# Kernel optimization log

Hardware: AMD Instinct MI355X
Metric: run time of the kernel (lower is better)

## Reference

```python
import jax, jax.numpy as jnp
import numpy as np

NUM_EMBEDDINGS = 8192
EMBEDDING_DIM = 256


def setup_inputs() -> dict:
    key = jax.random.key(0)
    k1, k2 = jax.random.split(key)
    z = jax.random.normal(k1, (16, EMBEDDING_DIM, 32, 32), dtype=jnp.float32)
    # nn.Embedding default init: N(0, 1)
    emb_table = jax.random.normal(k2, (NUM_EMBEDDINGS, EMBEDDING_DIM), dtype=jnp.float32)
    return {"z": z, "emb_table": emb_table}


def reference(z, emb_table):
    # z: [B, D, H, W]; emb_table: [K, D]
    B, D, H, W = z.shape
    # flatten to per-token vectors: [B*H*W, D]
    zf = z.reshape(B, D, H * W).transpose(0, 2, 1).reshape(B * H * W, D)
    Wt = jax.lax.stop_gradient(emb_table)  # original detaches W for distance
    # argmin of mean squared distance == argmin of squared distance;
    # expand ||z - w||^2 = ||z||^2 - 2 z.w + ||w||^2 (avoid (N,K,D) expansion)
    z_sq = jnp.sum(zf * zf, axis=-1, keepdims=True)          # [N, 1]
    w_sq = jnp.sum(Wt * Wt, axis=-1)                          # [K]
    dists = z_sq - 2.0 * (zf @ Wt.T) + w_sq                   # [N, K]
    token_ids = jnp.argmin(dists, axis=-1)                    # [N]
    quantized = emb_table[token_ids]                          # [N, D] (differentiable gather)
    return quantized.reshape(B, H * W, D).transpose(0, 2, 1).reshape(B, D, H, W)
```

## Files before the change

### kernel.cpp

```cpp
#include <hip/hip_runtime.h>
#include <stdint.h>

#define DIM 256
#define NEMB 8192
#define NTOK 16384
#define HW 1024

typedef __attribute__((ext_vector_type(4))) int int4v;

__device__ __forceinline__ void async_cp16(void* lds, const void* g) {
  __builtin_amdgcn_global_load_lds(
      (const __attribute__((address_space(1))) unsigned int*)g,
      (__attribute__((address_space(3))) unsigned int*)lds, 16, 0, 0);
}
__device__ __forceinline__ int q0_of(float x) {
  int q = __float2int_rn(x * 20.0f);
  return q > 127 ? 127 : (q < -127 ? -127 : q);
}
__device__ __forceinline__ int q1_of(float x, int q0) {
  float e = x * 20.0f - (float)q0;
  int q = __float2int_rn(e * 128.0f);
  return q > 127 ? 127 : (q < -127 ? -127 : q);
}
__device__ __forceinline__ unsigned int pack4(int a, int b, int c, int d) {
  return (unsigned int)(a & 0xff) | ((unsigned int)(b & 0xff) << 8) |
         ((unsigned int)(c & 0xff) << 16) | ((unsigned int)(d & 0xff) << 24);
}

__global__ __launch_bounds__(256) void prep_kernel(
    const float* __restrict__ emb, unsigned int* __restrict__ q0w,
    unsigned int* __restrict__ q1w, int* __restrict__ iwsq2,
    const float* __restrict__ z, unsigned int* __restrict__ q0z,
    unsigned int* __restrict__ q1z) {
  __shared__ float tile[64][65];
  int tid = threadIdx.x;
  int lane = tid & 63;
  if (blockIdx.x < 2048) {
    int row = blockIdx.x * 4 + (tid >> 6);
    const float4 v = *(const float4*)(emb + (size_t)row * DIM + lane * 4);
    float s = v.x * v.x + v.y * v.y + v.z * v.z + v.w * v.w;
    int a0 = q0_of(v.x), b0 = q0_of(v.y), c0 = q0_of(v.z), d0 = q0_of(v.w);
    q0w[row * (DIM / 4) + lane] = pack4(a0, b0, c0, d0);
    q1w[row * (DIM / 4) + lane] =
        pack4(q1_of(v.x, a0), q1_of(v.y, b0), q1_of(v.z, c0), q1_of(v.w, d0));
#pragma unroll
    for (int off = 32; off > 0; off >>= 1) s += __shfl_xor(s, off, 64);
    if (lane == 0) iwsq2[row] = (int)rintf(s * 25600.0f) + 8192;
    return;
  }
  int idx = blockIdx.x - 2048;
  int b = idx >> 6, d0 = ((idx >> 4) & 3) * 64, hw0 = (idx & 15) * 64;
  int grp = tid >> 6;
  const float* src = z + (size_t)b * DIM * HW + hw0 + lane;
#pragma unroll
  for (int i = 0; i < 16; i++) {
    int dl = grp + i * 4;
    tile[dl][lane] = src[(size_t)(d0 + dl) * HW];
  }
  __syncthreads();
  int dq = tid & 15;
#pragma unroll
  for (int p = 0; p < 4; p++) {
    int n = (tid >> 4) + p * 16;
    float x0 = tile[dq * 4 + 0][n], x1 = tile[dq * 4 + 1][n];
    float x2 = tile[dq * 4 + 2][n], x3 = tile[dq * 4 + 3][n];
    int a0 = q0_of(x0), b0 = q0_of(x1), c0 = q0_of(x2), e0 = q0_of(x3);
    int token = b * HW + hw0 + n;
    size_t off = (size_t)token * (DIM / 4) + (d0 >> 2) + dq;
    q0z[off] = pack4(a0, b0, c0, e0);
    q1z[off] = pack4(q1_of(x0, a0), q1_of(x1, b0), q1_of(x2, c0), q1_of(x3, e0));
  }
}

__global__ __launch_bounds__(128, 2) void gemm_topk_kernel(
    const signed char* __restrict__ q0z, const signed char* __restrict__ q1z,
    const signed char* __restrict__ q0w, const signed char* __restrict__ q1w,
    const int* __restrict__ iwsq2, uint2* __restrict__ partials) {
  __shared__ __align__(16) signed char sB[2][4][16 * 128];

  const int bid = blockIdx.x;
  const int kq = bid & 7;
  const int tg = bid >> 3;
  const int tid = threadIdx.x;
  const int lane = tid & 63, w = tid >> 6;
  const int c = lane & 15, quad = lane >> 4;
  const int n0 = tg * 128;
  const int k0g = kq * 1024;

  int4v af0[4][4], af1[4][4];
#pragma unroll
  for (int t = 0; t < 4; t++) {
    const size_t arow = (size_t)(n0 + w * 64 + t * 16 + c) * DIM;
#pragma unroll
    for (int s = 0; s < 4; s++) {
      af0[t][s] = *(const int4v*)(q0z + arow + s * 64 + quad * 16);
      af1[t][s] = *(const int4v*)(q1z + arow + s * 64 + quad * 16);
    }
  }

  const int srow = tid >> 3;
  const int scl = ((tid & 7) ^ (srow & 7)) * 16;
  const signed char* p0 = q0w + (size_t)(k0g + srow) * DIM + scl;
  const signed char* p1 = q1w + (size_t)(k0g + srow) * DIM + scl;
  async_cp16(&sB[0][0][tid * 16], p0);
  async_cp16(&sB[0][1][tid * 16], p0 + 128);
  async_cp16(&sB[0][2][tid * 16], p1);
  async_cp16(&sB[0][3][tid * 16], p1 + 128);
  p0 += 16 * DIM;
  p1 += 16 * DIM;
  __syncthreads();

  unsigned int m1[16], m2[16];
#pragma unroll
  for (int i = 0; i < 16; i++) { m1[i] = 0xFFFFFFFFu; m2[i] = 0xFFFFFFFFu; }

  unsigned int idx0 = (unsigned)(k0g + c);
  const int4v zero = {0, 0, 0, 0};

  for (int it = 0; it < 64; it++) {
    const int buf = it & 1;
    if (it + 1 < 64) {
      const int nb = buf ^ 1;
      async_cp16(&sB[nb][0][tid * 16], p0);
      async_cp16(&sB[nb][1][tid * 16], p0 + 128);
      async_cp16(&sB[nb][2][tid * 16], p1);
      async_cp16(&sB[nb][3][tid * 16], p1 + 128);
      p0 += 16 * DIM;
      p1 += 16 * DIM;
    }
    const int iw = iwsq2[k0g + it * 16 + c];

    int4v b0[4];
#pragma unroll
    for (int s = 0; s < 4; s++) {
      const int ph = ((((s & 1) << 2) + quad) ^ (c & 7)) * 16;
      b0[s] = *(const int4v*)(&sB[buf][s >> 1][c * 128 + ph]);
    }
    int4v a[4];
#pragma unroll
    for (int t = 0; t < 4; t++) {
      a[t] = __builtin_amdgcn_mfma_i32_16x16x64_i8(af0[t][0], b0[0], zero, 0, 0, 0);
#pragma unroll
      for (int s = 1; s < 4; s++)
        a[t] = __builtin_amdgcn_mfma_i32_16x16x64_i8(af0[t][s], b0[s], a[t], 0, 0, 0);
    }
#pragma unroll
    for (int t = 0; t < 4; t++)
#pragma unroll
      for (int r = 0; r < 4; r++) a[t][r] <<= 7;
#pragma unroll
    for (int t = 0; t < 4; t++)
#pragma unroll
      for (int s = 0; s < 4; s++)
        a[t] = __builtin_amdgcn_mfma_i32_16x16x64_i8(af1[t][s], b0[s], a[t], 0, 0, 0);
#pragma unroll
    for (int s = 0; s < 4; s++) {
      const int ph = ((((s & 1) << 2) + quad) ^ (c & 7)) * 16;
      int4v b1 = *(const int4v*)(&sB[buf][2 + (s >> 1)][c * 128 + ph]);
#pragma unroll
      for (int t = 0; t < 4; t++)
        a[t] = __builtin_amdgcn_mfma_i32_16x16x64_i8(af0[t][s], b1, a[t], 0, 0, 0);
    }
#pragma unroll
    for (int t = 0; t < 4; t++) {
#pragma unroll
      for (int r = 0; r < 4; r++) {
        unsigned int s0 = (unsigned int)(iw - a[t][r]);
        s0 = s0 < 0x2000000u ? s0 : 0x1FFFFFFu;
        unsigned int v = ((s0 << 7) & 0xFFFFE000u) | idx0;
        const int ix = t * 4 + r;
        unsigned int lo = v < m1[ix] ? v : m1[ix];
        unsigned int hi = v < m1[ix] ? m1[ix] : v;
        m2[ix] = m2[ix] < hi ? m2[ix] : hi;
        m1[ix] = lo;
      }
    }
    idx0 += 16;
    __syncthreads();
  }

#pragma unroll
  for (int ix = 0; ix < 16; ix++) {
    unsigned int a1m = m1[ix], a2m = m2[ix];
#pragma unroll
    for (int off = 1; off < 16; off <<= 1) {
      unsigned int o1 = __shfl_xor(a1m, off, 16);
      unsigned int o2 = __shfl_xor(a2m, off, 16);
      unsigned int n1 = a1m < o1 ? a1m : o1;
      unsigned int hi = a1m < o1 ? o1 : a1m;
      unsigned int l2 = a2m < o2 ? a2m : o2;
      a2m = hi < l2 ? hi : l2;
      a1m = n1;
    }
    m1[ix] = a1m;
    m2[ix] = a2m;
  }
  if (c == 0) {
#pragma unroll
    for (int t = 0; t < 4; t++) {
#pragma unroll
      for (int r = 0; r < 4; r++) {
        int token = n0 + w * 64 + t * 16 + quad * 4 + r;
        partials[(size_t)kq * NTOK + token] =
            make_uint2(m1[t * 4 + r], m2[t * 4 + r]);
      }
    }
  }
}

__global__ __launch_bounds__(256) void rescore_gather_kernel(
    const uint2* __restrict__ partials, const float* __restrict__ z,
    const float* __restrict__ emb, float* __restrict__ out) {
  __shared__ float tile[32][257];
  __shared__ int sid[32];
  const int b = blockIdx.x >> 5;
  const int hw0 = (blockIdx.x & 31) * 32;
  const int tid = threadIdx.x;
  const int w = tid >> 6, lane = tid & 63;
  for (int i = 0; i < 8; i++) {
    const int tl = w * 8 + i;
    const int token = b * HW + hw0 + tl;
    unsigned int p[16];
#pragma unroll
    for (int q = 0; q < 8; q++) {
      uint2 t = partials[(size_t)q * NTOK + token];
      p[q * 2] = t.x;
      p[q * 2 + 1] = t.y;
    }
    unsigned int smin = p[0];
#pragma unroll
    for (int q = 1; q < 16; q++) smin = p[q] < smin ? p[q] : smin;
    const unsigned int thr = (smin >> 13) + 64;
    int ns = 0;
#pragma unroll
    for (int q = 0; q < 16; q++) ns += ((p[q] >> 13) <= thr) ? 1 : 0;
    int chosen = (int)(smin & 0x1FFFu);
    if (ns > 1) {
      float zv[4];
#pragma unroll
      for (int j = 0; j < 4; j++)
        zv[j] = z[(size_t)b * DIM * HW + (size_t)(lane * 4 + j) * HW + hw0 + tl];
      double best = 1e300;
      int bid2 = NEMB;
#pragma unroll
      for (int q = 0; q < 16; q++) {
        if ((p[q] >> 13) <= thr) {
          int id = (int)(p[q] & 0x1FFFu);
          const float4 wv = *(const float4*)(emb + (size_t)id * DIM + lane * 4);
          double s = (double)wv.x * ((double)wv.x - 2.0 * (double)zv[0]) +
                     (double)wv.y * ((double)wv.y - 2.0 * (double)zv[1]) +
                     (double)wv.z * ((double)wv.z - 2.0 * (double)zv[2]) +
                     (double)wv.w * ((double)wv.w - 2.0 * (double)zv[3]);
#pragma unroll
          for (int off = 32; off > 0; off >>= 1) s += __shfl_xor(s, off, 64);
          if (s < best || (s == best && id < bid2)) {
            best = s;
            bid2 = id;
          }
        }
      }
      chosen = bid2;
    }
    if (lane == 0) sid[tl] = chosen;
  }
  __syncthreads();
  for (int i = 0; i < 32; i++)
    tile[i][tid] = emb[(size_t)sid[i] * DIM + tid];
  __syncthreads();
  int h = tid & 31, dg = tid >> 5;
  for (int i = 0; i < 32; i++) {
    int d = i * 8 + dg;
    out[(size_t)b * DIM * HW + (size_t)d * HW + hw0 + h] = tile[h][d];
  }
}

extern "C" void kernel_launch(void* const* d_in, const int* in_sizes, int n_in,
                              void* d_out, int out_size, void* d_ws, size_t ws_size,
                              hipStream_t stream) {
  const float* z = (const float*)d_in[0];
  const float* emb = (const float*)d_in[1];
  float* out = (float*)d_out;
  char* ws = (char*)d_ws;

  signed char* q0w = (signed char*)(ws);
  signed char* q1w = (signed char*)(ws + 2097152);
  signed char* q0z = (signed char*)(ws + 4194304);
  signed char* q1z = (signed char*)(ws + 8388608);
  int* iwsq2 = (int*)(ws + 12582912);
  uint2* partials = (uint2*)(ws + 12615680);

  prep_kernel<<<dim3(3072), 256, 0, stream>>>(
      emb, (unsigned int*)q0w, (unsigned int*)q1w, iwsq2, z, (unsigned int*)q0z,
      (unsigned int*)q1z);
  gemm_topk_kernel<<<dim3(1024), 128, 0, stream>>>(q0z, q1z, q0w, q1w, iwsq2,
                                                   partials);
  rescore_gather_kernel<<<dim3(512), 256, 0, stream>>>(partials, z, emb, out);
}
```

Before: 185.9 us.

## Retile GEMM-topk to 256 threads with 32-code tiles and compact rescoring

The GEMM-topk kernel moves to 256 threads per block. Each wave now owns 32 tokens and processes 32 codebook rows per iteration, with a doubled LDS tile, half as many loop iterations and fewer A-fragment registers, which is meant to raise occupancy and B reuse. The top-2 update uses v_med3_u32 on the minimum of two packed candidates, which cuts ALU work but keeps only one of each pair, so the runner-up tracking becomes approximate. The rescore kernel first screens all 32 tokens in parallel with 8 lanes each and builds a worklist, so full-wave double-precision rescoring runs only on ambiguous tokens.

```diff
diff --git a/kernel.cpp b/kernel.cpp
--- a/kernel.cpp
+++ b/kernel.cpp
@@ -25,6 +25,13 @@
 __device__ __forceinline__ unsigned int pack4(int a, int b, int c, int d) {
   return (unsigned int)(a & 0xff) | ((unsigned int)(b & 0xff) << 8) |
          ((unsigned int)(c & 0xff) << 16) | ((unsigned int)(d & 0xff) << 24);
+}
+__device__ __forceinline__ void top2_insert(unsigned int v, unsigned int& m1,
+                                            unsigned int& m2) {
+  unsigned int med;
+  asm("v_med3_u32 %0, %1, %2, %3" : "=v"(med) : "v"(v), "v"(m1), "v"(m2));
+  m2 = med;
+  m1 = v < m1 ? v : m1;
 }
 
 __global__ __launch_bounds__(256) void prep_kernel(
@@ -72,11 +79,11 @@
   }
 }
 
-__global__ __launch_bounds__(128, 2) void gemm_topk_kernel(
+__global__ __launch_bounds__(256, 3) void gemm_topk_kernel(
     const signed char* __restrict__ q0z, const signed char* __restrict__ q1z,
     const signed char* __restrict__ q0w, const signed char* __restrict__ q1w,
     const int* __restrict__ iwsq2, uint2* __restrict__ partials) {
-  __shared__ __align__(16) signed char sB[2][4][16 * 128];
+  __shared__ __align__(16) signed char sB[2][4][32 * 128];
 
   const int bid = blockIdx.x;
   const int kq = bid & 7;
@@ -87,10 +94,10 @@
   const int n0 = tg * 128;
   const int k0g = kq * 1024;
 
-  int4v af0[4][4], af1[4][4];
-#pragma unroll
-  for (int t = 0; t < 4; t++) {
-    const size_t arow = (size_t)(n0 + w * 64 + t * 16 + c) * DIM;
+  int4v af0[2][4], af1[2][4];
+#pragma unroll
+  for (int t = 0; t < 2; t++) {
+    const size_t arow = (size_t)(n0 + w * 32 + t * 16 + c) * DIM;
 #pragma unroll
     for (int s = 0; s < 4; s++) {
       af0[t][s] = *(const int4v*)(q0z + arow + s * 64 + quad * 16);
@@ -106,81 +113,92 @@
   async_cp16(&sB[0][1][tid * 16], p0 + 128);
   async_cp16(&sB[0][2][tid * 16], p1);
   async_cp16(&sB[0][3][tid * 16], p1 + 128);
-  p0 += 16 * DIM;
-  p1 += 16 * DIM;
-  __syncthreads();
-
-  unsigned int m1[16], m2[16];
-#pragma unroll
-  for (int i = 0; i < 16; i++) { m1[i] = 0xFFFFFFFFu; m2[i] = 0xFFFFFFFFu; }
-
-  unsigned int idx0 = (unsigned)(k0g + c);
+  p0 += 32 * DIM;
+  p1 += 32 * DIM;
+  __syncthreads();
+
+  unsigned int m1[8], m2[8];
+#pragma unroll
+  for (int i = 0; i < 8; i++) { m1[i] = 0xFFFFFFFFu; m2[i] = 0xFFFFFFFFu; }
+
+  unsigned int idxA = (unsigned)(k0g + c);
   const int4v zero = {0, 0, 0, 0};
 
-  for (int it = 0; it < 64; it++) {
+  for (int it = 0; it < 32; it++) {
     const int buf = it & 1;
-    if (it + 1 < 64) {
+    if (it + 1 < 32) {
       const int nb = buf ^ 1;
       async_cp16(&sB[nb][0][tid * 16], p0);
       async_cp16(&sB[nb][1][tid * 16], p0 + 128);
       async_cp16(&sB[nb][2][tid * 16], p1);
       async_cp16(&sB[nb][3][tid * 16], p1 + 128);
-      p0 += 16 * DIM;
-      p1 += 16 * DIM;
-    }
-    const int iw = iwsq2[k0g + it * 16 + c];
-
-    int4v b0[4];
+      p0 += 32 * DIM;
+      p1 += 32 * DIM;
+    }
+    const int iw0 = iwsq2[k0g + it * 32 + c];
+    const int iw1 = iwsq2[k0g + it * 32 + 16 + c];
+
+    int4v b0a[4], b0b[4];
 #pragma unroll
     for (int s = 0; s < 4; s++) {
       const int ph = ((((s & 1) << 2) + quad) ^ (c & 7)) * 16;
-      b0[s] = *(const int4v*)(&sB[buf][s >> 1][c * 128 + ph]);
-    }
-    int4v a[4];
-#pragma unroll
-    for (int t = 0; t < 4; t++) {
-      a[t] = __builtin_amdgcn_mfma_i32_16x16x64_i8(af0[t][0], b0[0], zero, 0, 0, 0);
-#pragma unroll
-      for (int s = 1; s < 4; s++)
-        a[t] = __builtin_amdgcn_mfma_i32_16x16x64_i8(af0[t][s], b0[s], a[t], 0, 0, 0);
-    }
-#pragma unroll
-    for (int t = 0; t < 4; t++)
-#pragma unroll
-      for (int r = 0; r < 4; r++) a[t][r] <<= 7;
-#pragma unroll
-    for (int t = 0; t < 4; t++)
-#pragma unroll
-      for (int s = 0; s < 4; s++)
-        a[t] = __builtin_amdgcn_mfma_i32_16x16x64_i8(af1[t][s], b0[s], a[t], 0, 0, 0);
+      b0a[s] = *(const int4v*)(&sB[buf][s >> 1][c * 128 + ph]);
+      b0b[s] = *(const int4v*)(&sB[buf][s >> 1][(16 + c) * 128 + ph]);
+    }
+    int4v a[2][2];
+#pragma unroll
+    for (int t = 0; t < 2; t++) {
+      a[t][0] = __builtin_amdgcn_mfma_i32_16x16x64_i8(af0[t][0], b0a[0], zero, 0, 0, 0);
+      a[t][1] = __builtin_amdgcn_mfma_i32_16x16x64_i8(af0[t][0], b0b[0], zero, 0, 0, 0);
+#pragma unroll
+      for (int s = 1; s < 4; s++) {
+        a[t][0] = __builtin_amdgcn_mfma_i32_16x16x64_i8(af0[t][s], b0a[s], a[t][0], 0, 0, 0);
+        a[t][1] = __builtin_amdgcn_mfma_i32_16x16x64_i8(af0[t][s], b0b[s], a[t][1], 0, 0, 0);
+      }
+    }
+#pragma unroll
+    for (int t = 0; t < 2; t++)
+#pragma unroll
+      for (int cn = 0; cn < 2; cn++)
+#pragma unroll
+        for (int r = 0; r < 4; r++) a[t][cn][r] <<= 7;
+#pragma unroll
+    for (int t = 0; t < 2; t++)
+#pragma unroll
+      for (int s = 0; s < 4; s++) {
+        a[t][0] = __builtin_amdgcn_mfma_i32_16x16x64_i8(af1[t][s], b0a[s], a[t][0], 0, 0, 0);
+        a[t][1] = __builtin_amdgcn_mfma_i32_16x16x64_i8(af1[t][s], b0b[s], a[t][1], 0, 0, 0);
+      }
 #pragma unroll
     for (int s = 0; s < 4; s++) {
       const int ph = ((((s & 1) << 2) + quad) ^ (c & 7)) * 16;
-      int4v b1 = *(const int4v*)(&sB[buf][2 + (s >> 1)][c * 128 + ph]);
-#pragma unroll
-      for (int t = 0; t < 4; t++)
-        a[t] = __builtin_amdgcn_mfma_i32_16x16x64_i8(af0[t][s], b1, a[t], 0, 0, 0);
-    }
-#pragma unroll
-    for (int t = 0; t < 4; t++) {
+      int4v b1a = *(const int4v*)(&sB[buf][2 + (s >> 1)][c * 128 + ph]);
+      int4v b1b = *(const int4v*)(&sB[buf][2 + (s >> 1)][(16 + c) * 128 + ph]);
+#pragma unroll
+      for (int t = 0; t < 2; t++) {
+        a[t][0] = __builtin_amdgcn_mfma_i32_16x16x64_i8(af0[t][s], b1a, a[t][0], 0, 0, 0);
+        a[t][1] = __builtin_amdgcn_mfma_i32_16x16x64_i8(af0[t][s], b1b, a[t][1], 0, 0, 0);
+      }
+    }
+#pragma unroll
+    for (int t = 0; t < 2; t++) {
 #pragma unroll
       for (int r = 0; r < 4; r++) {
-        unsigned int s0 = (unsigned int)(iw - a[t][r]);
+        unsigned int s0 = (unsigned int)(iw0 - a[t][0][r]);
+        unsigned int s1 = (unsigned int)(iw1 - a[t][1][r]);
         s0 = s0 < 0x2000000u ? s0 : 0x1FFFFFFu;
-        unsigned int v = ((s0 << 7) & 0xFFFFE000u) | idx0;
-        const int ix = t * 4 + r;
-        unsigned int lo = v < m1[ix] ? v : m1[ix];
-        unsigned int hi = v < m1[ix] ? m1[ix] : v;
-        m2[ix] = m2[ix] < hi ? m2[ix] : hi;
-        m1[ix] = lo;
-      }
-    }
-    idx0 += 16;
+        s1 = s1 < 0x2000000u ? s1 : 0x1FFFFFFu;
+        unsigned int pk0 = ((s0 << 7) & 0xFFFFE000u) | idxA;
+        unsigned int pk1 = ((s1 << 7) & 0xFFFFE000u) | (idxA + 16);
+        top2_insert(pk0 < pk1 ? pk0 : pk1, m1[t * 4 + r], m2[t * 4 + r]);
+      }
+    }
+    idxA += 32;
     __syncthreads();
   }
 
 #pragma unroll
-  for (int ix = 0; ix < 16; ix++) {
+  for (int ix = 0; ix < 8; ix++) {
     unsigned int a1m = m1[ix], a2m = m2[ix];
 #pragma unroll
     for (int off = 1; off < 16; off <<= 1) {
@@ -197,10 +215,10 @@
   }
   if (c == 0) {
 #pragma unroll
-    for (int t = 0; t < 4; t++) {
+    for (int t = 0; t < 2; t++) {
 #pragma unroll
       for (int r = 0; r < 4; r++) {
-        int token = n0 + w * 64 + t * 16 + quad * 4 + r;
+        int token = n0 + w * 32 + t * 16 + quad * 4 + r;
         partials[(size_t)kq * NTOK + token] =
             make_uint2(m1[t * 4 + r], m2[t * 4 + r]);
       }
@@ -213,29 +231,53 @@
     const float* __restrict__ emb, float* __restrict__ out) {
   __shared__ float tile[32][257];
   __shared__ int sid[32];
+  __shared__ int wl[32];
+  __shared__ int nwl;
   const int b = blockIdx.x >> 5;
   const int hw0 = (blockIdx.x & 31) * 32;
   const int tid = threadIdx.x;
-  const int w = tid >> 6, lane = tid & 63;
-  for (int i = 0; i < 8; i++) {
-    const int tl = w * 8 + i;
+  if (tid == 0) nwl = 0;
+  __syncthreads();
+  {
+    const int tl = tid >> 3, sub = tid & 7;
     const int token = b * HW + hw0 + tl;
-    unsigned int p[16];
-#pragma unroll
-    for (int q = 0; q < 8; q++) {
-      uint2 t = partials[(size_t)q * NTOK + token];
-      p[q * 2] = t.x;
-      p[q * 2 + 1] = t.y;
-    }
-    unsigned int smin = p[0];
-#pragma unroll
-    for (int q = 1; q < 16; q++) smin = p[q] < smin ? p[q] : smin;
-    const unsigned int thr = (smin >> 13) + 64;
-    int ns = 0;
-#pragma unroll
-    for (int q = 0; q < 16; q++) ns += ((p[q] >> 13) <= thr) ? 1 : 0;
-    int chosen = (int)(smin & 0x1FFFu);
-    if (ns > 1) {
+    uint2 e = partials[(size_t)sub * NTOK + token];
+    unsigned int m = e.x < e.y ? e.x : e.y;
+#pragma unroll
+    for (int off = 1; off < 8; off <<= 1) {
+      unsigned int o = __shfl_xor(m, off, 8);
+      m = o < m ? o : m;
+    }
+    const unsigned int thr = (m >> 13) + 64;
+    int cnt = (((e.x >> 13) <= thr) ? 1 : 0) + (((e.y >> 13) <= thr) ? 1 : 0);
+#pragma unroll
+    for (int off = 1; off < 8; off <<= 1) cnt += __shfl_xor(cnt, off, 8);
+    if (sub == 0) {
+      if (cnt == 1) {
+        sid[tl] = (int)(m & 0x1FFFu);
+      } else {
+        int i = atomicAdd(&nwl, 1);
+        wl[i] = tl;
+      }
+    }
+  }
+  __syncthreads();
+  {
+    const int w = tid >> 6, lane = tid & 63;
+    for (int i = w; i < nwl; i += 4) {
+      const int tl = wl[i];
+      const int token = b * HW + hw0 + tl;
+      unsigned int p[16];
+#pragma unroll
+      for (int q = 0; q < 8; q++) {
+        uint2 t = partials[(size_t)q * NTOK + token];
+        p[q * 2] = t.x;
+        p[q * 2 + 1] = t.y;
+      }
+      unsigned int smin = p[0];
+#pragma unroll
+      for (int q = 1; q < 16; q++) smin = p[q] < smin ? p[q] : smin;
+      const unsigned int thr = (smin >> 13) + 64;
       float zv[4];
 #pragma unroll
       for (int j = 0; j < 4; j++)
@@ -259,9 +301,8 @@
           }
         }
       }
-      chosen = bid2;
-    }
-    if (lane == 0) sid[tl] = chosen;
+      if (lane == 0) sid[tl] = bid2;
+    }
   }
   __syncthreads();
   for (int i = 0; i < 32; i++)
@@ -292,7 +333,7 @@
   prep_kernel<<<dim3(3072), 256, 0, stream>>>(
       emb, (unsigned int*)q0w, (unsigned int*)q1w, iwsq2, z, (unsigned int*)q0z,
       (unsigned int*)q1z);
-  gemm_topk_kernel<<<dim3(1024), 128, 0, stream>>>(q0z, q1z, q0w, q1w, iwsq2,
+  gemm_topk_kernel<<<dim3(1024), 256, 0, stream>>>(q0z, q1z, q0w, q1w, iwsq2,
                                                    partials);
   rescore_gather_kernel<<<dim3(512), 256, 0, stream>>>(partials, z, emb, out);
 }
```

After: 172.6 us. -7.1%, faster.
